# Performance work log

Measured on AMD Instinct MI355X. Metric: run time of the kernel, lower is better.

Reference implementation:

```python
import jax, jax.numpy as jnp
import numpy as np

NUM_HEADS = 16

def rotate_half(x):
    h = x.shape[-1] // 2
    return jnp.concatenate([-x[..., h:], x[..., :h]], axis=-1)

def setup_inputs() -> dict:
    key = jax.random.key(0)
    k1, k2, k3 = jax.random.split(key, 3)
    B, S, H = 2, 2048, 1024
    x = jax.random.normal(k1, (B, S, H), dtype=jnp.float32)
    W_qkv = jax.random.normal(k2, (3 * H, H), dtype=jnp.float32) * (1.0 / np.sqrt(H))
    W_proj = jax.random.normal(k3, (H, H), dtype=jnp.float32) * (1.0 / np.sqrt(H))
    return {"x": x, "W_qkv": W_qkv, "W_proj": W_proj}

def reference(x, W_qkv, W_proj):
    B, S, H = x.shape
    nH = NUM_HEADS
    hd = H // nH
    # QKV projection (bias=False): y = x @ W.T
    qkv = jnp.einsum('bsh,oh->bso', x, W_qkv)  # [B,S,3H]
    q, k, v = jnp.split(qkv, 3, axis=-1)
    def to_heads(t):
        return t.reshape(B, S, nH, hd).transpose(0, 2, 1, 3)  # [B,nH,S,hd]
    q, k, v = to_heads(q), to_heads(k), to_heads(v)
    # RoPE on first half of head_dim; freqs dim = hd//2
    half = hd // 2
    inv_freq = 1.0 / (10000.0 ** (jnp.arange(0, hd, 2, dtype=jnp.float32) / hd))  # [hd//2]
    t = jnp.arange(S, dtype=jnp.float32)
    freqs = t[:, None] * inv_freq[None, :]  # [S, hd//2]
    cos = jnp.cos(freqs)[None, None]  # [1,1,S,hd//2]
    sin = jnp.sin(freqs)[None, None]
    q_half, q_rest = q[..., :half], q[..., half:]
    k_half, k_rest = k[..., :half], k[..., half:]
    q_rot = q_half * cos + rotate_half(q_half) * sin
    k_rot = k_half * cos + rotate_half(k_half) * sin
    q = jnp.concatenate([q_rot, q_rest], axis=-1)
    k = jnp.concatenate([k_rot, k_rest], axis=-1)
    # scaled dot-product attention (no mask, dropout=0 / eval)
    scale = 1.0 / np.sqrt(hd)
    att = jnp.einsum('bhqd,bhkd->bhqk', q, k) * scale  # [B,nH,S,S]
    att = jax.nn.softmax(att, axis=-1)
    out = jnp.einsum('bhqk,bhkd->bhqd', att, v)  # [B,nH,S,hd]
    out = out.transpose(0, 2, 1, 3).reshape(B, S, H)
    return jnp.einsum('bsh,oh->bso', out, W_proj)
```

## Files before the change

kernel.cpp:

```cpp
#include <hip/hip_runtime.h>
#include <math.h>

#define SEQ  2048
#define NHD  16
#define HD   64
#define HDIM 1024

typedef short s16x8 __attribute__((ext_vector_type(8)));
typedef short s16x4 __attribute__((ext_vector_type(4)));
typedef float f32x4 __attribute__((ext_vector_type(4)));

typedef const __attribute__((address_space(1))) unsigned int* gp_t;
typedef __attribute__((address_space(3))) unsigned int* lp_t;

__device__ __forceinline__ void async16(const short* g, short* l) {
    __builtin_amdgcn_global_load_lds((gp_t)g, (lp_t)l, 16, 0, 0);
}

__device__ __forceinline__ short f2bf(float f) {
    unsigned int u = __float_as_uint(f);
    u += 0x7fff + ((u >> 16) & 1);
    return (short)(u >> 16);
}

__global__ void detect_k(const unsigned short* __restrict__ x, int* __restrict__ flag) {
    int cnt = 0;
    #pragma unroll 4
    for (int j = 0; j < 32; ++j) {
        unsigned short h = x[threadIdx.x * 32 + j];
        int e = (h >> 7) & 0xFF;
        cnt += (e >= 100 && e <= 140) ? 1 : 0;
    }
    __shared__ int tot;
    if (threadIdx.x == 0) tot = 0;
    __syncthreads();
    atomicAdd(&tot, cnt);
    __syncthreads();
    if (threadIdx.x == 0) *flag = (tot > (8192 * 9) / 10) ? 1 : 0;
}

#define XG4  (4096 * 1024 / 4)
#define WQG4 (3072 * 1024 / 4)
#define WPG4 (1024 * 1024 / 4)
__global__ void cvt_all_k(const void* __restrict__ xr, const void* __restrict__ wqr,
                          const void* __restrict__ wpr, short* __restrict__ xo,
                          short* __restrict__ wqo, short* __restrict__ wpo,
                          const int* __restrict__ flag) {
    int i = blockIdx.x * 256 + threadIdx.x;
    const void* in; short* out; int j;
    if (i < XG4)             { in = xr;  out = xo;  j = i; }
    else if (i < XG4 + WQG4) { in = wqr; out = wqo; j = i - XG4; }
    else                     { in = wpr; out = wpo; j = i - XG4 - WQG4; }
    if (*flag) {
        ((s16x4*)out)[j] = ((const s16x4*)in)[j];
    } else {
        f32x4 v = ((const f32x4*)in)[j];
        s16x4 r;
        r[0] = f2bf(v[0]); r[1] = f2bf(v[1]);
        r[2] = f2bf(v[2]); r[3] = f2bf(v[3]);
        ((s16x4*)out)[j] = r;
    }
}

__global__ void rope_tab_k(float2* __restrict__ tab) {
    int i = blockIdx.x * 256 + threadIdx.x;
    if (i >= SEQ * 32) return;
    int s = i >> 5, d = i & 31;
    float invf = (float)pow(10000.0, -(double)d / 32.0);
    float af = (float)s * invf;
    double a = (double)af;
    tab[i] = make_float2((float)cos(a), (float)sin(a));
}

template<int MODE>
__global__ __launch_bounds__(256, 2)
void gemm_bt(const short* __restrict__ A, const short* __restrict__ B,
             short* __restrict__ q, short* __restrict__ kbuf, short* __restrict__ vt,
             float* __restrict__ C, const float2* __restrict__ tab,
             int K, int N) {
    __shared__ __align__(16) short As[128 * 32];
    __shared__ __align__(16) short Bs[128 * 32];
    const int tid  = threadIdx.x;
    const int w    = tid >> 6, lane = tid & 63;
    const int quad = lane >> 4, l16 = lane & 15;
    const int wm = (w >> 1) * 64, wn = (w & 1) * 64;
    const int rowA0 = blockIdx.y * 128;
    const int colB0 = blockIdx.x * 128;

    f32x4 acc[4][4] = {};

    for (int kb = 0; kb < K; kb += 32) {
        __syncthreads();
        #pragma unroll
        for (int i = 0; i < 2; ++i) {
            int cidx = i * 256 + w * 64 + lane;
            int row = cidx >> 2, sc = cidx & 3;
            int c = sc ^ (row & 3);
            async16(&A[(long)(rowA0 + row) * K + kb + c * 8],
                    &As[(i * 256 + w * 64) * 8]);
            async16(&B[(long)(colB0 + row) * K + kb + c * 8],
                    &Bs[(i * 256 + w * 64) * 8]);
        }
        __syncthreads();

        s16x8 af[4], bfr[4];
        const int slot = quad ^ (l16 & 3);
        #pragma unroll
        for (int mi = 0; mi < 4; ++mi)
            af[mi] = *(const s16x8*)&As[(wm + mi * 16 + l16) * 32 + slot * 8];
        #pragma unroll
        for (int ni = 0; ni < 4; ++ni)
            bfr[ni] = *(const s16x8*)&Bs[(wn + ni * 16 + l16) * 32 + slot * 8];
        #pragma unroll
        for (int mi = 0; mi < 4; ++mi)
            #pragma unroll
            for (int ni = 0; ni < 4; ++ni)
                acc[mi][ni] = __builtin_amdgcn_mfma_f32_16x16x32_bf16(
                    af[mi], bfr[ni], acc[mi][ni], 0, 0, 0);
    }

    const int cb = colB0 + wn;
    if (MODE == 1) {
        #pragma unroll
        for (int mi = 0; mi < 4; ++mi) {
            #pragma unroll
            for (int r = 0; r < 4; ++r) {
                int gm = rowA0 + wm + mi * 16 + quad * 4 + r;
                float* cp = C + (long)gm * N + cb + l16;
                #pragma unroll
                for (int ni = 0; ni < 4; ++ni)
                    cp[ni * 16] = acc[mi][ni][r];
            }
        }
        return;
    }
    const int sector = cb >> 10;
    const int head   = (cb & 1023) >> 6;
    if (sector < 2) {
        const float sc = (sector == 0) ? 0.125f : 1.0f;
        #pragma unroll
        for (int mi = 0; mi < 4; ++mi) {
            #pragma unroll
            for (int r = 0; r < 4; ++r) {
                int gm = rowA0 + wm + mi * 16 + quad * 4 + r;
                int b = gm >> 11, s = gm & 2047;
                float v0 = acc[mi][0][r], v1 = acc[mi][1][r];
                float v2 = acc[mi][2][r], v3 = acc[mi][3][r];
                float2 cs0 = tab[s * 32 + l16];
                float2 cs1 = tab[s * 32 + 16 + l16];
                float n0 = v0 * cs0.x - v1 * cs0.y;
                float n1 = v1 * cs1.x + v0 * cs1.y;
                short* dst = (sector == 0 ? q : kbuf)
                           + ((long)((b * NHD + head) * SEQ + s)) * HD + l16;
                dst[0]  = f2bf(n0 * sc);  dst[16] = f2bf(n1 * sc);
                dst[32] = f2bf(v2 * sc);  dst[48] = f2bf(v3 * sc);
            }
        }
    } else {
        #pragma unroll
        for (int mi = 0; mi < 4; ++mi) {
            int srow = rowA0 + wm + mi * 16 + quad * 4;
            int b = srow >> 11, s0 = srow & 2047;
            #pragma unroll
            for (int ni = 0; ni < 4; ++ni) {
                s16x4 pk;
                #pragma unroll
                for (int r = 0; r < 4; ++r) pk[r] = f2bf(acc[mi][ni][r]);
                *(s16x4*)&vt[((long)((b * NHD + head) * HD + ni * 16 + l16)) * SEQ + s0] = pk;
            }
        }
    }
}

__global__ __launch_bounds__(256, 2)
void flash_attn(const short* __restrict__ Q, const short* __restrict__ K,
                const short* __restrict__ Vt, short* __restrict__ O) {
    __shared__ __align__(16) short Qs[128 * 64];
    __shared__ __align__(16) short Ks[64 * 64];
    __shared__ __align__(16) short Vs[64 * 64];
    const int tid  = threadIdx.x;
    const int w    = tid >> 6, lane = tid & 63;
    const int quad = lane >> 4, l16 = lane & 15;
    const int bh = blockIdx.y;
    const int qb = blockIdx.x * 128;
    const short* Qp = Q  + (long)bh * SEQ * HD + (long)qb * HD;
    const short* Kp = K  + (long)bh * SEQ * HD;
    const short* Vp = Vt + (long)bh * HD * SEQ;

    #pragma unroll
    for (int i = 0; i < 4; ++i) {
        int cidx = i * 256 + w * 64 + lane;
        int row = cidx >> 3, sc = cidx & 7;
        int c = sc ^ (row & 7);
        async16(&Qp[row * HD + c * 8], &Qs[(i * 256 + w * 64) * 8]);
    }
    __syncthreads();
    s16x8 aq[2][2];
    #pragma unroll
    for (int mi = 0; mi < 2; ++mi)
        #pragma unroll
        for (int ks = 0; ks < 2; ++ks)
            aq[mi][ks] = *(const s16x8*)&Qs[(w * 32 + mi * 16 + l16) * 64
                                            + ((ks * 4 + quad) ^ (l16 & 7)) * 8];

    s16x8 ones4 = {};
    #pragma unroll
    for (int j = 0; j < 4; ++j) ones4[j] = (short)0x3F80;

    float m_i[2] = {-1e30f, -1e30f};
    f32x4 oacc[2][4] = {};
    f32x4 lacc[2] = {};

    for (int kt = 0; kt < SEQ / 64; ++kt) {
        __syncthreads();
        #pragma unroll
        for (int i = 0; i < 2; ++i) {
            int cidx = i * 256 + w * 64 + lane;
            int row = cidx >> 3, sc = cidx & 7;
            int c = sc ^ (row & 7);
            async16(&Kp[(kt * 64 + row) * HD + c * 8], &Ks[(i * 256 + w * 64) * 8]);
            async16(&Vp[(long)row * SEQ + kt * 64 + c * 8], &Vs[(i * 256 + w * 64) * 8]);
        }
        __syncthreads();

        f32x4 st[2][4] = {};
        #pragma unroll
        for (int ki = 0; ki < 4; ++ki) {
            s16x8 ak0 = *(const s16x8*)&Ks[(ki * 16 + l16) * 64 + (quad ^ (l16 & 7)) * 8];
            s16x8 ak1 = *(const s16x8*)&Ks[(ki * 16 + l16) * 64 + ((4 + quad) ^ (l16 & 7)) * 8];
            #pragma unroll
            for (int mi = 0; mi < 2; ++mi) {
                st[mi][ki] = __builtin_amdgcn_mfma_f32_16x16x32_bf16(
                    ak0, aq[mi][0], st[mi][ki], 0, 0, 0);
                st[mi][ki] = __builtin_amdgcn_mfma_f32_16x16x32_bf16(
                    ak1, aq[mi][1], st[mi][ki], 0, 0, 0);
            }
        }

        s16x8 bp[2][4];
        #pragma unroll
        for (int mi = 0; mi < 2; ++mi) {
            float mx = st[mi][0][0];
            #pragma unroll
            for (int ki = 0; ki < 4; ++ki)
                #pragma unroll
                for (int r = 0; r < 4; ++r) mx = fmaxf(mx, st[mi][ki][r]);
            mx = fmaxf(mx, __shfl_xor(mx, 16));
            mx = fmaxf(mx, __shfl_xor(mx, 32));
            float mn = fmaxf(m_i[mi], mx);
            float alpha = __expf(m_i[mi] - mn);
            m_i[mi] = mn;
            #pragma unroll
            for (int ki = 0; ki < 4; ++ki) {
                s16x8 f = {};
                #pragma unroll
                for (int r = 0; r < 4; ++r)
                    f[r] = f2bf(__expf(st[mi][ki][r] - mn));
                bp[mi][ki] = f;
            }
            #pragma unroll
            for (int nd = 0; nd < 4; ++nd) oacc[mi][nd] *= alpha;
            lacc[mi] *= alpha;
        }

        #pragma unroll
        for (int ki = 0; ki < 4; ++ki) {
            #pragma unroll
            for (int nd = 0; nd < 4; ++nd) {
                int d = nd * 16 + l16;
                s16x4 v4 = *(const s16x4*)&Vs[d * 64
                             + ((ki * 2 + (quad >> 1)) ^ (l16 & 7)) * 8
                             + (quad & 1) * 4];
                s16x8 av = {v4[0], v4[1], v4[2], v4[3], 0, 0, 0, 0};
                #pragma unroll
                for (int mi = 0; mi < 2; ++mi)
                    oacc[mi][nd] = __builtin_amdgcn_mfma_f32_16x16x32_bf16(
                        av, bp[mi][ki], oacc[mi][nd], 0, 0, 0);
            }
            #pragma unroll
            for (int mi = 0; mi < 2; ++mi)
                lacc[mi] = __builtin_amdgcn_mfma_f32_16x16x32_bf16(
                    ones4, bp[mi][ki], lacc[mi], 0, 0, 0);
        }
    }

    const int b = bh >> 4, h = bh & 15;
    #pragma unroll
    for (int mi = 0; mi < 2; ++mi) {
        int srow = qb + w * 32 + mi * 16 + l16;
        float inv = 1.0f / lacc[mi][0];
        short* op = O + ((long)(b * SEQ + srow) * HDIM) + h * HD + quad * 4;
        #pragma unroll
        for (int nd = 0; nd < 4; ++nd) {
            s16x4 pk;
            #pragma unroll
            for (int r = 0; r < 4; ++r) pk[r] = f2bf(oacc[mi][nd][r] * inv);
            *(s16x4*)&op[nd * 16] = pk;
        }
    }
}

extern "C" void kernel_launch(void* const* d_in, const int* in_sizes, int n_in,
                              void* d_out, int out_size, void* d_ws, size_t ws_size,
                              hipStream_t stream) {
    const void* x_raw  = d_in[0];
    const void* Wq_raw = d_in[1];
    const void* Wp_raw = d_in[2];
    for (int i = 0; i < n_in; ++i) {
        if      (in_sizes[i] == 4096 * 1024) x_raw  = d_in[i];
        else if (in_sizes[i] == 3072 * 1024) Wq_raw = d_in[i];
        else if (in_sizes[i] == 1024 * 1024) Wp_raw = d_in[i];
    }
    float* out = (float*)d_out;

    const size_t MB = 1u << 20;
    char* ws = (char*)d_ws;
    short*  q    = (short*)(ws);
    short*  k    = (short*)(ws +  8 * MB);
    short*  vt   = (short*)(ws + 16 * MB);
    short*  xbf  = (short*)(ws + 24 * MB);
    short*  att  = xbf;
    short*  wqkv = (short*)(ws + 32 * MB);
    short*  wprj = (short*)(ws + 38 * MB);
    float2* tab  = (float2*)(ws + 40 * MB);
    int*    flag = (int*)(ws + 40 * MB + 512 * 1024);

    detect_k<<<dim3(1), dim3(256), 0, stream>>>((const unsigned short*)x_raw, flag);

    cvt_all_k<<<dim3((XG4 + WQG4 + WPG4) / 256), dim3(256), 0, stream>>>(
        x_raw, Wq_raw, Wp_raw, xbf, wqkv, wprj, flag);

    rope_tab_k<<<dim3(SEQ * 32 / 256), dim3(256), 0, stream>>>(tab);

    gemm_bt<0><<<dim3(3072 / 128, 4096 / 128), dim3(256), 0, stream>>>(
        xbf, wqkv, q, k, vt, (float*)nullptr, tab, 1024, 3072);

    flash_attn<<<dim3(SEQ / 128, 2 * NHD), dim3(256), 0, stream>>>(q, k, vt, att);

    gemm_bt<1><<<dim3(1024 / 128, 4096 / 128), dim3(256), 0, stream>>>(
        att, wprj, (short*)nullptr, (short*)nullptr, (short*)nullptr, out, tab, 1024, 1024);
}
```

Measured before the change: 221.6 us.

## Split flash attention over KV halves and merge partials; use full-K PV MFMAs

Flash attention now launches a third grid dimension that splits the key sequence into two halves, writing unnormalized bf16 partial outputs plus per-row max and sum to workspace. A new merge kernel combines the two halves with log-sum-exp weights and writes the attention output. The PV and row-sum MFMAs also pack two 16-key chunks into one K=32 instruction instead of zero-padding half of it, halving those MFMA counts. The split doubles grid size from 512 blocks to improve CU occupancy, at the cost of an extra launch, extra global traffic, and bf16 rounding of unnormalized partials.

```diff
diff --git a/kernel.cpp b/kernel.cpp
--- a/kernel.cpp
+++ b/kernel.cpp
@@ -21,6 +21,9 @@
     unsigned int u = __float_as_uint(f);
     u += 0x7fff + ((u >> 16) & 1);
     return (short)(u >> 16);
+}
+__device__ __forceinline__ float bf2f(short s) {
+    return __uint_as_float(((unsigned int)(unsigned short)s) << 16);
 }
 
 __global__ void detect_k(const unsigned short* __restrict__ x, int* __restrict__ flag) {
@@ -174,7 +177,8 @@
 
 __global__ __launch_bounds__(256, 2)
 void flash_attn(const short* __restrict__ Q, const short* __restrict__ K,
-                const short* __restrict__ Vt, short* __restrict__ O) {
+                const short* __restrict__ Vt, short* __restrict__ opart,
+                float2* __restrict__ mlpart) {
     __shared__ __align__(16) short Qs[128 * 64];
     __shared__ __align__(16) short Ks[64 * 64];
     __shared__ __align__(16) short Vs[64 * 64];
@@ -183,6 +187,7 @@
     const int quad = lane >> 4, l16 = lane & 15;
     const int bh = blockIdx.y;
     const int qb = blockIdx.x * 128;
+    const int z  = blockIdx.z;
     const short* Qp = Q  + (long)bh * SEQ * HD + (long)qb * HD;
     const short* Kp = K  + (long)bh * SEQ * HD;
     const short* Vp = Vt + (long)bh * HD * SEQ;
@@ -203,15 +208,15 @@
             aq[mi][ks] = *(const s16x8*)&Qs[(w * 32 + mi * 16 + l16) * 64
                                             + ((ks * 4 + quad) ^ (l16 & 7)) * 8];
 
-    s16x8 ones4 = {};
-    #pragma unroll
-    for (int j = 0; j < 4; ++j) ones4[j] = (short)0x3F80;
+    s16x8 ones8;
+    #pragma unroll
+    for (int j = 0; j < 8; ++j) ones8[j] = (short)0x3F80;
 
     float m_i[2] = {-1e30f, -1e30f};
     f32x4 oacc[2][4] = {};
     f32x4 lacc[2] = {};
 
-    for (int kt = 0; kt < SEQ / 64; ++kt) {
+    for (int kt = z * 16; kt < z * 16 + 16; ++kt) {
         __syncthreads();
         #pragma unroll
         for (int i = 0; i < 2; ++i) {
@@ -237,7 +242,7 @@
             }
         }
 
-        s16x8 bp[2][4];
+        s16x8 bp[2][2];
         #pragma unroll
         for (int mi = 0; mi < 2; ++mi) {
             float mx = st[mi][0][0];
@@ -251,12 +256,14 @@
             float alpha = __expf(m_i[mi] - mn);
             m_i[mi] = mn;
             #pragma unroll
-            for (int ki = 0; ki < 4; ++ki) {
-                s16x8 f = {};
-                #pragma unroll
-                for (int r = 0; r < 4; ++r)
-                    f[r] = f2bf(__expf(st[mi][ki][r] - mn));
-                bp[mi][ki] = f;
+            for (int t = 0; t < 2; ++t) {
+                s16x8 f;
+                #pragma unroll
+                for (int r = 0; r < 4; ++r) {
+                    f[r]     = f2bf(__expf(st[mi][2 * t][r] - mn));
+                    f[4 + r] = f2bf(__expf(st[mi][2 * t + 1][r] - mn));
+                }
+                bp[mi][t] = f;
             }
             #pragma unroll
             for (int nd = 0; nd < 4; ++nd) oacc[mi][nd] *= alpha;
@@ -264,40 +271,67 @@
         }
 
         #pragma unroll
-        for (int ki = 0; ki < 4; ++ki) {
+        for (int t = 0; t < 2; ++t) {
             #pragma unroll
             for (int nd = 0; nd < 4; ++nd) {
                 int d = nd * 16 + l16;
-                s16x4 v4 = *(const s16x4*)&Vs[d * 64
-                             + ((ki * 2 + (quad >> 1)) ^ (l16 & 7)) * 8
+                s16x4 va = *(const s16x4*)&Vs[d * 64
+                             + ((4 * t + (quad >> 1)) ^ (l16 & 7)) * 8
                              + (quad & 1) * 4];
-                s16x8 av = {v4[0], v4[1], v4[2], v4[3], 0, 0, 0, 0};
+                s16x4 vb = *(const s16x4*)&Vs[d * 64
+                             + ((4 * t + 2 + (quad >> 1)) ^ (l16 & 7)) * 8
+                             + (quad & 1) * 4];
+                s16x8 av = {va[0], va[1], va[2], va[3],
+                            vb[0], vb[1], vb[2], vb[3]};
                 #pragma unroll
                 for (int mi = 0; mi < 2; ++mi)
                     oacc[mi][nd] = __builtin_amdgcn_mfma_f32_16x16x32_bf16(
-                        av, bp[mi][ki], oacc[mi][nd], 0, 0, 0);
+                        av, bp[mi][t], oacc[mi][nd], 0, 0, 0);
             }
             #pragma unroll
             for (int mi = 0; mi < 2; ++mi)
                 lacc[mi] = __builtin_amdgcn_mfma_f32_16x16x32_bf16(
-                    ones4, bp[mi][ki], lacc[mi], 0, 0, 0);
-        }
-    }
-
-    const int b = bh >> 4, h = bh & 15;
+                    ones8, bp[mi][t], lacc[mi], 0, 0, 0);
+        }
+    }
+
     #pragma unroll
     for (int mi = 0; mi < 2; ++mi) {
         int srow = qb + w * 32 + mi * 16 + l16;
-        float inv = 1.0f / lacc[mi][0];
-        short* op = O + ((long)(b * SEQ + srow) * HDIM) + h * HD + quad * 4;
+        long prow = (long)(z * 32 + bh) * SEQ + srow;
+        if (quad == 0) mlpart[prow] = make_float2(m_i[mi], lacc[mi][0]);
+        short* op = opart + prow * 64 + quad * 4;
         #pragma unroll
         for (int nd = 0; nd < 4; ++nd) {
             s16x4 pk;
             #pragma unroll
-            for (int r = 0; r < 4; ++r) pk[r] = f2bf(oacc[mi][nd][r] * inv);
+            for (int r = 0; r < 4; ++r) pk[r] = f2bf(oacc[mi][nd][r]);
             *(s16x4*)&op[nd * 16] = pk;
         }
     }
+}
+
+__global__ __launch_bounds__(256)
+void merge_k(const short* __restrict__ opart, const float2* __restrict__ mlpart,
+             short* __restrict__ att) {
+    int idx = blockIdx.x * 256 + threadIdx.x;
+    int t16 = idx & 15, rowg = idx >> 4;
+    int bh = rowg >> 11, srow = rowg & 2047;
+    float2 ml1 = mlpart[rowg];
+    float2 ml2 = mlpart[65536 + rowg];
+    float m  = fmaxf(ml1.x, ml2.x);
+    float w1 = __expf(ml1.x - m), w2 = __expf(ml2.x - m);
+    float inv = 1.0f / (w1 * ml1.y + w2 * ml2.y);
+    w1 *= inv; w2 *= inv;
+    s16x4 o1 = *(const s16x4*)&opart[(long)rowg * 64 + t16 * 4];
+    s16x4 o2 = *(const s16x4*)&opart[(long)(65536 + rowg) * 64 + t16 * 4];
+    int b = bh >> 4, h = bh & 15;
+    short* dst = att + ((long)(b * SEQ + srow)) * HDIM + h * HD + t16 * 4;
+    s16x4 r;
+    #pragma unroll
+    for (int j = 0; j < 4; ++j)
+        r[j] = f2bf(w1 * bf2f(o1[j]) + w2 * bf2f(o2[j]));
+    *(s16x4*)dst = r;
 }
 
 extern "C" void kernel_launch(void* const* d_in, const int* in_sizes, int n_in,
@@ -315,15 +349,17 @@
 
     const size_t MB = 1u << 20;
     char* ws = (char*)d_ws;
-    short*  q    = (short*)(ws);
-    short*  k    = (short*)(ws +  8 * MB);
-    short*  vt   = (short*)(ws + 16 * MB);
-    short*  xbf  = (short*)(ws + 24 * MB);
-    short*  att  = xbf;
-    short*  wqkv = (short*)(ws + 32 * MB);
-    short*  wprj = (short*)(ws + 38 * MB);
-    float2* tab  = (float2*)(ws + 40 * MB);
-    int*    flag = (int*)(ws + 40 * MB + 512 * 1024);
+    short*  q     = (short*)(ws);
+    short*  k     = (short*)(ws +  8 * MB);
+    short*  vt    = (short*)(ws + 16 * MB);
+    short*  xbf   = (short*)(ws + 24 * MB);
+    short*  att   = xbf;
+    short*  wqkv  = (short*)(ws + 32 * MB);
+    short*  wprj  = (short*)(ws + 38 * MB);
+    float2* tab   = (float2*)(ws + 40 * MB);
+    int*    flag  = (int*)(ws + 40 * MB + 512 * 1024);
+    short*  opart = (short*)(ws + 41 * MB);
+    float2* mlprt = (float2*)(ws + 57 * MB);
 
     detect_k<<<dim3(1), dim3(256), 0, stream>>>((const unsigned short*)x_raw, flag);
 
@@ -335,7 +371,10 @@
     gemm_bt<0><<<dim3(3072 / 128, 4096 / 128), dim3(256), 0, stream>>>(
         xbf, wqkv, q, k, vt, (float*)nullptr, tab, 1024, 3072);
 
-    flash_attn<<<dim3(SEQ / 128, 2 * NHD), dim3(256), 0, stream>>>(q, k, vt, att);
+    flash_attn<<<dim3(SEQ / 128, 2 * NHD, 2), dim3(256), 0, stream>>>(
+        q, k, vt, opart, mlprt);
+
+    merge_k<<<dim3(65536 * 16 / 256), dim3(256), 0, stream>>>(opart, mlprt, att);
 
     gemm_bt<1><<<dim3(1024 / 128, 4096 / 128), dim3(256), 0, stream>>>(
         att, wprj, (short*)nullptr, (short*)nullptr, (short*)nullptr, out, tab, 1024, 1024);
```

Result: faster. 205.9 us (-7.1%).
